# Optimization experiments

Hardware: AMD Instinct MI355X
Metric: run time of the kernel (lower is better)

Reference implementation:

```python
import jax, jax.numpy as jnp
from jax import lax
import numpy as np

D_MODEL = 768
D_STATE = 64
D_CONV = 4
EXPAND = 2
HEADDIM = 128
NGROUPS = 1
D_INNER = EXPAND * D_MODEL            # 1536
NHEADS = D_INNER // HEADDIM           # 12
D_IN_PROJ = 2 * D_INNER + 2 * NGROUPS * D_STATE + NHEADS  # 3212
CONV_DIM = D_INNER + 2 * NGROUPS * D_STATE                # 1664
BATCH, SEQLEN = 2, 4096
EPS = 1e-5


def setup_inputs() -> dict:
    key = jax.random.key(0)
    ks = jax.random.split(key, 8)
    u = jax.random.normal(ks[0], (BATCH, SEQLEN, D_MODEL), jnp.float32)
    W_in = jax.random.normal(ks[1], (D_IN_PROJ, D_MODEL), jnp.float32) * 0.02
    conv_w = jax.random.normal(ks[2], (CONV_DIM, D_CONV), jnp.float32) * 0.2
    conv_b = jnp.zeros((CONV_DIM,), jnp.float32)
    # dt_bias init as in BaseMambaBlock: inv-softplus of dt ~ logU(dt_min, dt_max)
    dt = jnp.exp(jax.random.uniform(ks[3], (NHEADS,)) * (np.log(0.1) - np.log(0.001)) + np.log(0.001))
    dt = jnp.clip(dt, 1e-4, None)
    dt_bias = dt + jnp.log(-jnp.expm1(-dt))
    A_log = jnp.log(jnp.abs(jax.random.normal(ks[4], (NHEADS,), jnp.float32)))
    Dp = jnp.ones((NHEADS,), jnp.float32)
    norm_w = jnp.ones((D_INNER,), jnp.float32)
    W_out = jax.random.normal(ks[5], (D_MODEL, D_INNER), jnp.float32) * 0.02
    return dict(u=u, W_in=W_in, conv_w=conv_w, conv_b=conv_b, dt_bias=dt_bias,
                A_log=A_log, Dp=Dp, norm_w=norm_w, W_out=W_out)


def _silu(x):
    return x * jax.nn.sigmoid(x)


def _depthwise_causal_conv(x, w, b):
    # x: [B, L, C], w: [C, W], b: [C]. Causal: left-pad W-1, crop to L.
    Bt, L, C = x.shape
    xp = jnp.pad(x, ((0, 0), (D_CONV - 1, 0), (0, 0)))
    # stack D_CONV shifted views: [B, L, C, W]
    taps = jnp.stack([xp[:, k:k + L, :] for k in range(D_CONV)], axis=-1)
    return jnp.einsum('blcw,cw->blc', taps, w) + b


def reference(u, W_in, conv_w, conv_b, dt_bias, A_log, Dp, norm_w, W_out):
    Bt, L, _ = u.shape
    zxbcdt = jnp.einsum('bld,ed->ble', u, W_in)  # [B, L, 3212]
    z = zxbcdt[..., :D_INNER]                                   # [B,L,1536]
    xBC = zxbcdt[..., D_INNER:D_INNER + CONV_DIM]               # [B,L,1664]
    dt = zxbcdt[..., D_INNER + CONV_DIM:]                       # [B,L,H]
    dt = jax.nn.softplus(dt + dt_bias)                          # [B,L,H]

    xBC = _silu(_depthwise_causal_conv(xBC, conv_w, conv_b))
    x = xBC[..., :D_INNER].reshape(Bt, L, NHEADS, HEADDIM)      # [B,L,H,P]
    Bm = xBC[..., D_INNER:D_INNER + NGROUPS * D_STATE]          # [B,L,N] (ngroups=1)
    Cm = xBC[..., D_INNER + NGROUPS * D_STATE:]                 # [B,L,N]

    A = -jnp.exp(A_log)                                         # [H]
    dA = jnp.exp(dt * A)                                        # [B,L,H]

    # time-major scan over the selective-state-space recurrence
    xs = (jnp.swapaxes(x, 0, 1),   # [L,B,H,P]
          jnp.swapaxes(dt, 0, 1),  # [L,B,H]
          jnp.swapaxes(dA, 0, 1),  # [L,B,H]
          jnp.swapaxes(Bm, 0, 1),  # [L,B,N]
          jnp.swapaxes(Cm, 0, 1))  # [L,B,N]

    def step(state, inp):
        x_t, dt_t, dA_t, B_t, C_t = inp
        # state: [B,H,P,N]
        state = state * dA_t[..., None, None] + (dt_t[..., None] * x_t)[..., None] * B_t[:, None, None, :]
        y_t = jnp.einsum('bhpn,bn->bhp', state, C_t)
        return state, y_t

    state0 = jnp.zeros((Bt, NHEADS, HEADDIM, D_STATE), u.dtype)
    _, y = lax.scan(step, state0, xs)                           # y: [L,B,H,P]
    y = jnp.swapaxes(y, 0, 1) + Dp[None, None, :, None] * x     # skip term D*x
    y = y.reshape(Bt, L, D_INNER)

    # RMSNormGated, norm_before_gate=False: normalize(y * silu(z)) * weight
    g = y * _silu(z)
    g = g * jax.lax.rsqrt(jnp.mean(g * g, axis=-1, keepdims=True) + EPS) * norm_w
    return jnp.einsum('bli,di->bld', g, W_out)
```

## Files before the change

### kernel.cpp

```cpp
#include <hip/hip_runtime.h>
#include <hip/hip_bf16.h>
#include <stdint.h>

#define BATCH   2
#define SEQLEN  4096
#define DMODEL  768
#define DSTATE  64
#define DCONV   4
#define HEADDIM 128
#define NHEADS  12
#define DINNER  1536
#define DINPROJ 3212
#define CONVDIM 1664
#define DXBC    1676
#define NPAD1   3328
#define ROWS    (BATCH*SEQLEN)
#define CHUNK   64
#define NCHUNK  (SEQLEN/CHUNK)
#define CROWS   8
#define TBUF    4096

typedef __bf16 bf16x8 __attribute__((ext_vector_type(8)));
typedef float  f32x4  __attribute__((ext_vector_type(4)));

__device__ __forceinline__ f32x4 splat4(float v) { return (f32x4){v, v, v, v}; }

__device__ __forceinline__ void load_lds16(const void* g, void* l) {
    __builtin_amdgcn_global_load_lds(
        (const __attribute__((address_space(1))) unsigned int*)g,
        (__attribute__((address_space(3))) unsigned int*)l, 16, 0, 0);
}

__global__ void cvt_bf16_kernel(const float* __restrict__ src,
                                __hip_bfloat16* __restrict__ dst, int n) {
    int i = (blockIdx.x * blockDim.x + threadIdx.x) * 4;
    if (i + 3 < n) {
        float4 v = *(const float4*)(src + i);
        dst[i + 0] = __float2bfloat16(v.x);
        dst[i + 1] = __float2bfloat16(v.y);
        dst[i + 2] = __float2bfloat16(v.z);
        dst[i + 3] = __float2bfloat16(v.w);
    } else {
        for (; i < n; ++i) dst[i] = __float2bfloat16(src[i]);
    }
}

__global__ void padw1_kernel(const float* __restrict__ src,
                             __hip_bfloat16* __restrict__ dst) {
    int i = blockIdx.x * blockDim.x + threadIdx.x;
    if (i >= NPAD1 * DMODEL) return;
    int r = i / DMODEL;
    float v = (r < DINPROJ) ? src[i] : 0.f;
    dst[i] = __float2bfloat16(v);
}

__global__ __launch_bounds__(256) void gemm_bf16_nt(
    const __hip_bfloat16* __restrict__ A,
    const __hip_bfloat16* __restrict__ Bt,
    float* __restrict__ C,
    int M, int Nreal, int K, int ldc)
{
    __shared__ __align__(16) __hip_bfloat16 As[2 * TBUF];
    __shared__ __align__(16) __hip_bfloat16 Bs[2 * TBUF];
    const int tid  = threadIdx.x;
    const int lane = tid & 63;
    const int wave = tid >> 6;
    const int wm   = wave >> 1;
    const int wn   = wave & 1;
    const int tm   = blockIdx.x * 128;
    const int tn   = blockIdx.y * 128;

    f32x4 acc[4][4] = {};

    const int lrow = tid >> 2;
    const int lk8s = ((tid & 3) * 8) ^ (((tid >> 3) & 3) << 3);
    const __hip_bfloat16* gA0 = A  + (size_t)(tm + lrow)      * K + lk8s;
    const __hip_bfloat16* gA1 = A  + (size_t)(tm + lrow + 64) * K + lk8s;
    const __hip_bfloat16* gB0 = Bt + (size_t)(tn + lrow)      * K + lk8s;
    const __hip_bfloat16* gB1 = Bt + (size_t)(tn + lrow + 64) * K + lk8s;

    const int fr  = lane & 15;
    const int fks = ((lane >> 4) * 8) ^ (((lane >> 1) & 3) << 3);

    load_lds16(gA0, As + tid * 8);
    load_lds16(gA1, As + tid * 8 + 2048);
    load_lds16(gB0, Bs + tid * 8);
    load_lds16(gB1, Bs + tid * 8 + 2048);
    __syncthreads();

    int bufo = 0;
    for (int kk = 0; kk < K; kk += 32) {
        const int nbufo = bufo ^ TBUF;
        if (kk + 32 < K) {
            load_lds16(gA0 + kk + 32, As + nbufo + tid * 8);
            load_lds16(gA1 + kk + 32, As + nbufo + tid * 8 + 2048);
            load_lds16(gB0 + kk + 32, Bs + nbufo + tid * 8);
            load_lds16(gB1 + kk + 32, Bs + nbufo + tid * 8 + 2048);
        }
        bf16x8 af[4], bfr[4];
#pragma unroll
        for (int i = 0; i < 4; ++i) {
            af[i]  = *(const bf16x8*)(As + bufo + (wm * 64 + i * 16 + fr) * 32 + fks);
            bfr[i] = *(const bf16x8*)(Bs + bufo + (wn * 64 + i * 16 + fr) * 32 + fks);
        }
#pragma unroll
        for (int mi = 0; mi < 4; ++mi)
#pragma unroll
            for (int ni = 0; ni < 4; ++ni)
                acc[mi][ni] = __builtin_amdgcn_mfma_f32_16x16x32_bf16(
                    af[mi], bfr[ni], acc[mi][ni], 0, 0, 0);
        __syncthreads();
        bufo = nbufo;
    }

    const int rq = (lane >> 4) * 4;
#pragma unroll
    for (int mi = 0; mi < 4; ++mi) {
#pragma unroll
        for (int ni = 0; ni < 4; ++ni) {
            int col = tn + wn * 64 + ni * 16 + fr;
            if (col < Nreal) {
                size_t rbase = (size_t)(tm + wm * 64 + mi * 16 + rq) * ldc + col;
#pragma unroll
                for (int j = 0; j < 4; ++j)
                    C[rbase + (size_t)j * ldc] = acc[mi][ni][j];
            }
        }
    }
}

__global__ __launch_bounds__(256) void gemm1_fused(
    const __hip_bfloat16* __restrict__ A,
    const __hip_bfloat16* __restrict__ Bt,
    float* __restrict__ Cz,
    float* __restrict__ Cx)
{
    __shared__ __align__(16) __hip_bfloat16 As[2 * TBUF];
    __shared__ __align__(16) __hip_bfloat16 Bs[2 * TBUF];
    const int tid  = threadIdx.x;
    const int lane = tid & 63;
    const int wave = tid >> 6;
    const int wm   = wave >> 1;
    const int wn   = wave & 1;
    const int tm   = blockIdx.x * 128;
    const int tn   = blockIdx.y * 128;
    const int K    = DMODEL;

    float* Co;
    int ldc2, cb, nb;
    if (tn < DINNER) { Co = Cz; ldc2 = DINNER; cb = tn;          nb = DINNER; }
    else             { Co = Cx; ldc2 = DXBC;   cb = tn - DINNER; nb = DXBC;   }

    f32x4 acc[4][4] = {};

    const int lrow = tid >> 2;
    const int lk8s = ((tid & 3) * 8) ^ (((tid >> 3) & 3) << 3);
    const __hip_bfloat16* gA0 = A  + (size_t)(tm + lrow)      * K + lk8s;
    const __hip_bfloat16* gA1 = A  + (size_t)(tm + lrow + 64) * K + lk8s;
    const __hip_bfloat16* gB0 = Bt + (size_t)(tn + lrow)      * K + lk8s;
    const __hip_bfloat16* gB1 = Bt + (size_t)(tn + lrow + 64) * K + lk8s;

    const int fr  = lane & 15;
    const int fks = ((lane >> 4) * 8) ^ (((lane >> 1) & 3) << 3);

    load_lds16(gA0, As + tid * 8);
    load_lds16(gA1, As + tid * 8 + 2048);
    load_lds16(gB0, Bs + tid * 8);
    load_lds16(gB1, Bs + tid * 8 + 2048);
    __syncthreads();

    int bufo = 0;
    for (int kk = 0; kk < K; kk += 32) {
        const int nbufo = bufo ^ TBUF;
        if (kk + 32 < K) {
            load_lds16(gA0 + kk + 32, As + nbufo + tid * 8);
            load_lds16(gA1 + kk + 32, As + nbufo + tid * 8 + 2048);
            load_lds16(gB0 + kk + 32, Bs + nbufo + tid * 8);
            load_lds16(gB1 + kk + 32, Bs + nbufo + tid * 8 + 2048);
        }
        bf16x8 af[4], bfr[4];
#pragma unroll
        for (int i = 0; i < 4; ++i) {
            af[i]  = *(const bf16x8*)(As + bufo + (wm * 64 + i * 16 + fr) * 32 + fks);
            bfr[i] = *(const bf16x8*)(Bs + bufo + (wn * 64 + i * 16 + fr) * 32 + fks);
        }
#pragma unroll
        for (int mi = 0; mi < 4; ++mi)
#pragma unroll
            for (int ni = 0; ni < 4; ++ni)
                acc[mi][ni] = __builtin_amdgcn_mfma_f32_16x16x32_bf16(
                    af[mi], bfr[ni], acc[mi][ni], 0, 0, 0);
        __syncthreads();
        bufo = nbufo;
    }

    const int rq = (lane >> 4) * 4;
#pragma unroll
    for (int mi = 0; mi < 4; ++mi) {
#pragma unroll
        for (int ni = 0; ni < 4; ++ni) {
            int col = cb + wn * 64 + ni * 16 + fr;
            if (col < nb) {
                size_t rbase = (size_t)(tm + wm * 64 + mi * 16 + rq) * ldc2 + col;
#pragma unroll
                for (int j = 0; j < 4; ++j)
                    Co[rbase + (size_t)j * ldc2] = acc[mi][ni][j];
            }
        }
    }
}

__global__ void conv_kernel(const float* __restrict__ xbcdt,
                            const float* __restrict__ convw,
                            const float* __restrict__ convb,
                            float* __restrict__ xbuf,
                            float* __restrict__ Bm,
                            float* __restrict__ Cm)
{
    int c = blockIdx.x * 256 + threadIdx.x;
    if (c >= CONVDIM) return;
    size_t row0 = (size_t)blockIdx.y * CROWS;
    int l0 = (int)(row0 & (SEQLEN - 1));
    float w0 = convw[c * 4 + 0];
    float w1 = convw[c * 4 + 1];
    float w2 = convw[c * 4 + 2];
    float w3 = convw[c * 4 + 3];
    float bias = convb[c];
    const float* src = xbcdt + row0 * DXBC + c;
    float x0 = (l0 >= 3) ? src[-3 * DXBC] : 0.f;
    float x1 = (l0 >= 2) ? src[-2 * DXBC] : 0.f;
    float x2 = (l0 >= 1) ? src[-1 * DXBC] : 0.f;
#pragma unroll
    for (int r = 0; r < CROWS; ++r) {
        float x3 = src[(size_t)r * DXBC];
        float acc = bias + x0 * w0 + x1 * w1 + x2 * w2 + x3 * w3;
        float v = acc / (1.f + __expf(-acc));
        size_t row = row0 + r;
        if (c < DINNER)               xbuf[row * DINNER + c] = v;
        else if (c < DINNER + DSTATE) Bm[row * DSTATE + (c - DINNER)] = v;
        else                          Cm[row * DSTATE + (c - DINNER - DSTATE)] = v;
        x0 = x1; x1 = x2; x2 = x3;
    }
}

__global__ void dt_kernel(const float* __restrict__ xbcdt,
                          const float* __restrict__ dt_bias,
                          const float* __restrict__ A_log,
                          float* __restrict__ dtb, float* __restrict__ dAb)
{
    int i = blockIdx.x * 256 + threadIdx.x;
    if (i >= ROWS * NHEADS) return;
    int row = i / NHEADS, h = i - row * NHEADS;
    float v = xbcdt[(size_t)row * DXBC + CONVDIM + h] + dt_bias[h];
    float dt = (v > 20.f) ? v : log1pf(__expf(v));
    float A = -__expf(A_log[h]);
    dtb[i] = dt;
    dAb[i] = __expf(dt * A);
}

__global__ __launch_bounds__(256) void chunk_state_f32(
    const float* __restrict__ xbuf, const float* __restrict__ Bm,
    const float* __restrict__ dtb, const float* __restrict__ dAb,
    float* __restrict__ Sloc, float* __restrict__ Pk)
{
    const int blk = blockIdx.x;
    const int k   = blk % NCHUNK;
    const int bh  = blk / NCHUNK;
    const int h   = bh % NHEADS;
    const int b   = bh / NHEADS;
    const int tid = threadIdx.x;
    const int pg  = tid >> 3;
    const int n0  = (tid & 7) * 8;
    const size_t row0 = (size_t)b * SEQLEN + k * CHUNK;
    const float* xbase = xbuf + (row0 * NHEADS + h) * HEADDIM + pg * 4;

    __shared__ __align__(16) float lB[CHUNK][DSTATE];
    __shared__ float lDA[CHUNK];
    __shared__ float ldt[CHUNK];

    for (int i = tid; i < CHUNK * DSTATE / 4; i += 256)
        ((float4*)&lB[0][0])[i] = ((const float4*)(Bm + row0 * DSTATE))[i];
    if (tid < CHUNK) {
        lDA[tid] = dAb[(row0 + tid) * NHEADS + h];
        ldt[tid] = dtb[(row0 + tid) * NHEADS + h];
    }
    __syncthreads();

    f32x4 s4[4][2] = {};
    f32x4 xt0[4], xt1[4];

#pragma unroll
    for (int tt = 0; tt < 4; ++tt)
        xt0[tt] = *(const f32x4*)(xbase + (size_t)tt * (NHEADS * HEADDIM));

#pragma unroll
    for (int tile = 0; tile < 16; ++tile) {
        f32x4* cur = (tile & 1) ? xt1 : xt0;
        f32x4* nxt = (tile & 1) ? xt0 : xt1;
        if (tile < 15) {
#pragma unroll
            for (int tt = 0; tt < 4; ++tt)
                nxt[tt] = *(const f32x4*)(xbase +
                    (size_t)((tile + 1) * 4 + tt) * (NHEADS * HEADDIM));
        }
#pragma unroll
        for (int tt = 0; tt < 4; ++tt) {
            int t = tile * 4 + tt;
            f32x4 da4 = splat4(lDA[t]);
            float dtv = ldt[t];
            f32x4 bv0 = *(const f32x4*)&lB[t][n0];
            f32x4 bv1 = *(const f32x4*)&lB[t][n0 + 4];
#pragma unroll
            for (int pl = 0; pl < 4; ++pl) {
                f32x4 dtx = splat4(dtv * cur[tt][pl]);
                s4[pl][0] = s4[pl][0] * da4 + dtx * bv0;
                s4[pl][1] = s4[pl][1] * da4 + dtx * bv1;
            }
        }
    }

    const size_t kbase = (size_t)(bh * NCHUNK + k) * (HEADDIM * DSTATE);
#pragma unroll
    for (int pl = 0; pl < 4; ++pl) {
        size_t a = kbase + (size_t)(pg * 4 + pl) * DSTATE + n0;
        *(f32x4*)(Sloc + a)     = s4[pl][0];
        *(f32x4*)(Sloc + a + 4) = s4[pl][1];
    }

    if (tid == 0) {
        float pr = 1.f;
#pragma unroll 8
        for (int t = 0; t < CHUNK; ++t) pr *= lDA[t];
        Pk[bh * NCHUNK + k] = pr;
    }
}

__global__ __launch_bounds__(256) void scan_phase2(
    float* __restrict__ Sloc, const float* __restrict__ Pk)
{
    int bh = blockIdx.x >> 5;
    int eo = (blockIdx.x & 31) * 256 + threadIdx.x;
    __shared__ float lP[NCHUNK];
    if (threadIdx.x < NCHUNK) lP[threadIdx.x] = Pk[bh * NCHUNK + threadIdx.x];
    __syncthreads();
    float s = 0.f;
    size_t base = (size_t)bh * NCHUNK * 8192 + eo;
#pragma unroll 8
    for (int k = 0; k < NCHUNK; ++k) {
        size_t a = base + (size_t)k * 8192;
        float f = Sloc[a];
        Sloc[a] = s;
        s = s * lP[k] + f;
    }
}

__global__ __launch_bounds__(256) void chunk_y_f32(
    const float* __restrict__ xbuf, const float* __restrict__ Bm,
    const float* __restrict__ Cm, const float* __restrict__ dtb,
    const float* __restrict__ dAb, const float* __restrict__ Dp,
    const float* __restrict__ Sini, float* __restrict__ ybuf)
{
    const int blk = blockIdx.x;
    const int kp  = blk % (NCHUNK / 2);
    const int bh  = blk / (NCHUNK / 2);
    const int h   = bh % NHEADS;
    const int b   = bh / NHEADS;
    const int tid = threadIdx.x;
    const int sub = tid >> 7;
    const int t2  = tid & 127;
    const int pg  = t2 >> 2;
    const int q   = t2 & 3;
    const int n0  = q * 16;
    const size_t prow0 = (size_t)b * SEQLEN + (size_t)kp * 2 * CHUNK;
    const size_t row0  = prow0 + (size_t)sub * CHUNK;
    const float* xbase = xbuf + (row0 * NHEADS + h) * HEADDIM + pg * 4;
    float* ybase = ybuf + (row0 * NHEADS + h) * HEADDIM + pg * 4;

    __shared__ __align__(16) float lB[64][DSTATE];
    __shared__ __align__(16) float lC[64][DSTATE];
    __shared__ float lDA[2 * CHUNK];
    __shared__ float ldt[2 * CHUNK];

    if (tid < 2 * CHUNK) {
        lDA[tid] = dAb[(prow0 + tid) * NHEADS + h];
        ldt[tid] = dtb[(prow0 + tid) * NHEADS + h];
    }

    f32x4 s4[4][4];
    const size_t kbase = (size_t)(bh * NCHUNK + kp * 2 + sub) * (HEADDIM * DSTATE);
#pragma unroll
    for (int pl = 0; pl < 4; ++pl) {
        size_t a = kbase + (size_t)(pg * 4 + pl) * DSTATE + n0;
#pragma unroll
        for (int nq = 0; nq < 4; ++nq)
            s4[pl][nq] = *(const f32x4*)(Sini + a + nq * 4);
    }
    const float dph = Dp[h];

#pragma unroll
    for (int w = 0; w < 2; ++w) {
        for (int i = tid; i < 64 * DSTATE / 4; i += 256) {
            int r  = i >> 4;
            int c4 = i & 15;
            size_t gr = prow0 + (size_t)(r >> 5) * CHUNK + w * 32 + (r & 31);
            ((float4*)&lB[r][0])[c4] = ((const float4*)(Bm + gr * DSTATE))[c4];
            ((float4*)&lC[r][0])[c4] = ((const float4*)(Cm + gr * DSTATE))[c4];
        }
        __syncthreads();

        f32x4 xt0[4], xt1[4];
#pragma unroll
        for (int tt = 0; tt < 4; ++tt)
            xt0[tt] = *(const f32x4*)(xbase + (size_t)(w * 32 + tt) * (NHEADS * HEADDIM));

#pragma unroll
        for (int tile = 0; tile < 8; ++tile) {
            f32x4* cur = (tile & 1) ? xt1 : xt0;
            f32x4* nxt = (tile & 1) ? xt0 : xt1;
            if (tile < 7) {
#pragma unroll
                for (int tt = 0; tt < 4; ++tt)
                    nxt[tt] = *(const f32x4*)(xbase +
                        (size_t)(w * 32 + (tile + 1) * 4 + tt) * (NHEADS * HEADDIM));
            }
#pragma unroll
            for (int tt = 0; tt < 4; ++tt) {
                int t  = w * 32 + tile * 4 + tt;
                int tr = sub * 32 + tile * 4 + tt;
                f32x4 da4 = splat4(lDA[sub * CHUNK + t]);
                float dtv = ldt[sub * CHUNK + t];
                f32x4 bv0 = *(const f32x4*)&lB[tr][n0];
                f32x4 bv1 = *(const f32x4*)&lB[tr][n0 + 4];
                f32x4 bv2 = *(const f32x4*)&lB[tr][n0 + 8];
                f32x4 bv3 = *(const f32x4*)&lB[tr][n0 + 12];
                f32x4 cv0 = *(const f32x4*)&lC[tr][n0];
                f32x4 cv1 = *(const f32x4*)&lC[tr][n0 + 4];
                f32x4 cv2 = *(const f32x4*)&lC[tr][n0 + 8];
                f32x4 cv3 = *(const f32x4*)&lC[tr][n0 + 12];
                float yr[4];
#pragma unroll
                for (int pl = 0; pl < 4; ++pl) {
                    f32x4 dtx = splat4(dtv * cur[tt][pl]);
                    f32x4 v0 = s4[pl][0] * da4 + dtx * bv0;
                    f32x4 v1 = s4[pl][1] * da4 + dtx * bv1;
                    f32x4 v2 = s4[pl][2] * da4 + dtx * bv2;
                    f32x4 v3 = s4[pl][3] * da4 + dtx * bv3;
                    s4[pl][0] = v0; s4[pl][1] = v1; s4[pl][2] = v2; s4[pl][3] = v3;
                    f32x4 y4 = cv0 * v0 + cv1 * v1 + cv2 * v2 + cv3 * v3;
                    float y = (y4[0] + y4[1]) + (y4[2] + y4[3]);
                    y += __shfl_xor(y, 1);
                    y += __shfl_xor(y, 2);
                    yr[pl] = y;
                }
                if (q == 0) {
                    f32x4 wv = {yr[0] + dph * cur[tt][0], yr[1] + dph * cur[tt][1],
                                yr[2] + dph * cur[tt][2], yr[3] + dph * cur[tt][3]};
                    *(f32x4*)(ybase + (size_t)t * (NHEADS * HEADDIM)) = wv;
                }
            }
        }
        if (w == 0) __syncthreads();
    }
}

#define NT 64
__global__ __launch_bounds__(256) void scan_kernel(
    const float* __restrict__ xbuf, const float* __restrict__ Bm,
    const float* __restrict__ Cm, const float* __restrict__ dtb,
    const float* __restrict__ dAb, const float* __restrict__ Dp,
    float* __restrict__ ybuf)
{
    int blk = blockIdx.x;
    int ps = blk & 7;
    int h  = (blk >> 3) % NHEADS;
    int b  = blk / (NHEADS * 8);
    int p0 = ps * 16;
    int tid = threadIdx.x;
    int pl  = tid >> 4;
    int n0  = (tid & 15) * 4;

    __shared__ __align__(16) float lB[NT][64];
    __shared__ __align__(16) float lC[NT][64];
    __shared__ __align__(16) float lDtx[NT][16];
    __shared__ float lDA[NT];
    __shared__ float lY[NT][16];

    float s0 = 0.f, s1 = 0.f, s2 = 0.f, s3 = 0.f;
    float dph = Dp[h];
    size_t rowbase = (size_t)b * SEQLEN;

    for (int t0 = 0; t0 < SEQLEN; t0 += NT) {
        for (int i = tid; i < NT * 64 / 4; i += 256) {
            ((float4*)&lB[0][0])[i] = ((const float4*)Bm)[(rowbase + t0) * 16 + i];
            ((float4*)&lC[0][0])[i] = ((const float4*)Cm)[(rowbase + t0) * 16 + i];
        }
        for (int i = tid; i < NT * 16; i += 256) {
            int t = i >> 4, pp = i & 15;
            size_t r = rowbase + t0 + t;
            lDtx[t][pp] = dtb[r * NHEADS + h] * xbuf[(r * NHEADS + h) * HEADDIM + p0 + pp];
        }
        if (tid < NT) lDA[tid] = dAb[(rowbase + t0 + tid) * NHEADS + h];
        __syncthreads();

        for (int t = 0; t < NT; ++t) {
            float da  = lDA[t];
            float dtx = lDtx[t][pl];
            const float* bp = &lB[t][n0];
            const float* cp = &lC[t][n0];
            s0 = s0 * da + dtx * bp[0];
            s1 = s1 * da + dtx * bp[1];
            s2 = s2 * da + dtx * bp[2];
            s3 = s3 * da + dtx * bp[3];
            float part = s0 * cp[0] + s1 * cp[1] + s2 * cp[2] + s3 * cp[3];
            part += __shfl_xor(part, 1);
            part += __shfl_xor(part, 2);
            part += __shfl_xor(part, 4);
            part += __shfl_xor(part, 8);
            if ((tid & 15) == 0) lY[t][pl] = part;
        }
        __syncthreads();

        for (int i = tid; i < NT * 16; i += 256) {
            int t = i >> 4, pp = i & 15;
            size_t r = rowbase + t0 + t;
            size_t gi = (r * NHEADS + h) * HEADDIM + p0 + pp;
            ybuf[gi] = lY[t][pp] + dph * xbuf[gi];
        }
        __syncthreads();
    }
}

__global__ __launch_bounds__(256) void gate_rms_kernel(
    const float* __restrict__ ybuf, const float* __restrict__ zbuf,
    const float* __restrict__ norm_w, __hip_bfloat16* __restrict__ gbf)
{
    int row = blockIdx.x;
    int tid = threadIdx.x;
    const float2* y2 = (const float2*)(ybuf + (size_t)row * DINNER);
    const float2* z2 = (const float2*)(zbuf + (size_t)row * DINNER);
    const float2* nw2 = (const float2*)norm_w;
    float g[6];
    float ss = 0.f;
#pragma unroll
    for (int j = 0; j < 3; ++j) {
        int idx = tid + j * 256;
        float2 yy = y2[idx];
        float2 zz = z2[idx];
        float g0 = yy.x * (zz.x / (1.f + __expf(-zz.x)));
        float g1 = yy.y * (zz.y / (1.f + __expf(-zz.y)));
        g[j * 2 + 0] = g0;
        g[j * 2 + 1] = g1;
        ss += g0 * g0 + g1 * g1;
    }
#pragma unroll
    for (int m = 1; m < 64; m <<= 1) ss += __shfl_xor(ss, m);
    __shared__ float red[4];
    if ((tid & 63) == 0) red[tid >> 6] = ss;
    __syncthreads();
    float tot = red[0] + red[1] + red[2] + red[3];
    float scale = rsqrtf(tot * (1.f / DINNER) + 1e-5f);
#pragma unroll
    for (int j = 0; j < 3; ++j) {
        int idx = tid + j * 256;
        float2 w = nw2[idx];
        __hip_bfloat162 o;
        o.x = __float2bfloat16(g[j * 2 + 0] * scale * w.x);
        o.y = __float2bfloat16(g[j * 2 + 1] * scale * w.y);
        *(__hip_bfloat162*)(gbf + (size_t)row * DINNER + idx * 2) = o;
    }
}

extern "C" void kernel_launch(void* const* d_in, const int* in_sizes, int n_in,
                              void* d_out, int out_size, void* d_ws, size_t ws_size,
                              hipStream_t stream)
{
    const float* u       = (const float*)d_in[0];
    const float* W_in    = (const float*)d_in[1];
    const float* conv_w  = (const float*)d_in[2];
    const float* conv_b  = (const float*)d_in[3];
    const float* dt_bias = (const float*)d_in[4];
    const float* A_log   = (const float*)d_in[5];
    const float* Dp      = (const float*)d_in[6];
    const float* norm_w  = (const float*)d_in[7];
    const float* W_out   = (const float*)d_in[8];
    float* out = (float*)d_out;

    char* ws = (char*)d_ws;
    size_t off = 0;
    auto alloc = [&](size_t bytes) {
        char* p = ws + off;
        off += (bytes + 255) & ~(size_t)255;
        return p;
    };
    __hip_bfloat16* ubf  = (__hip_bfloat16*)alloc((size_t)ROWS * DMODEL * 2);
    __hip_bfloat16* W1bf = (__hip_bfloat16*)alloc((size_t)NPAD1 * DMODEL * 2);
    __hip_bfloat16* W2bf = (__hip_bfloat16*)alloc((size_t)DMODEL * DINNER * 2);
    float* zbuf  = (float*)alloc((size_t)ROWS * DINNER * 4);
    float* xbcdt = (float*)alloc((size_t)ROWS * DXBC * 4);
    float* xbuf = (float*)alloc((size_t)ROWS * DINNER * 4);
    float* Bmb  = (float*)alloc((size_t)ROWS * DSTATE * 4);
    float* Cmb  = (float*)alloc((size_t)ROWS * DSTATE * 4);
    float* dtb  = (float*)alloc((size_t)ROWS * NHEADS * 4);
    float* dAb  = (float*)alloc((size_t)ROWS * NHEADS * 4);
    float* ybuf = (float*)alloc((size_t)ROWS * DINNER * 4);
    float* Pkb  = (float*)alloc((size_t)BATCH * NHEADS * NCHUNK * 4);
    __hip_bfloat16* gbf = (__hip_bfloat16*)xbuf;
    float* Sloc = (float*)xbcdt;
    bool chunked = (off <= ws_size);

    cvt_bf16_kernel<<<(ROWS * DMODEL / 4 + 255) / 256, 256, 0, stream>>>(u, ubf, ROWS * DMODEL);
    padw1_kernel<<<(NPAD1 * DMODEL + 255) / 256, 256, 0, stream>>>(W_in, W1bf);
    cvt_bf16_kernel<<<(DMODEL * DINNER / 4 + 255) / 256, 256, 0, stream>>>(W_out, W2bf, DMODEL * DINNER);

    gemm1_fused<<<dim3(ROWS / 128, NPAD1 / 128), 256, 0, stream>>>(
        ubf, W1bf, zbuf, xbcdt);

    conv_kernel<<<dim3((CONVDIM + 255) / 256, ROWS / CROWS), 256, 0, stream>>>(
        xbcdt, conv_w, conv_b, xbuf, Bmb, Cmb);

    dt_kernel<<<(ROWS * NHEADS + 255) / 256, 256, 0, stream>>>(xbcdt, dt_bias, A_log, dtb, dAb);

    if (chunked) {
        chunk_state_f32<<<BATCH * NHEADS * NCHUNK, 256, 0, stream>>>(
            xbuf, Bmb, dtb, dAb, Sloc, Pkb);
        scan_phase2<<<BATCH * NHEADS * 32, 256, 0, stream>>>(Sloc, Pkb);
        chunk_y_f32<<<BATCH * NHEADS * NCHUNK / 2, 256, 0, stream>>>(
            xbuf, Bmb, Cmb, dtb, dAb, Dp, Sloc, ybuf);
    } else {
        scan_kernel<<<BATCH * NHEADS * 8, 256, 0, stream>>>(
            xbuf, Bmb, Cmb, dtb, dAb, Dp, ybuf);
    }

    gate_rms_kernel<<<ROWS, 256, 0, stream>>>(ybuf, zbuf, norm_w, gbf);

    gemm_bf16_nt<<<dim3(ROWS / 128, DMODEL / 128), 256, 0, stream>>>(
        gbf, W2bf, out, ROWS, DMODEL, DINNER, DMODEL);
}
```

Measured before the change: 305.3 us.

## Fuse dt computation into conv kernel and give each chunk its own block in chunk_y

```diff
diff --git a/kernel.cpp b/kernel.cpp
--- a/kernel.cpp
+++ b/kernel.cpp
@@ -213,49 +213,52 @@
 __global__ void conv_kernel(const float* __restrict__ xbcdt,
                             const float* __restrict__ convw,
                             const float* __restrict__ convb,
+                            const float* __restrict__ dt_bias,
+                            const float* __restrict__ A_log,
                             float* __restrict__ xbuf,
                             float* __restrict__ Bm,
-                            float* __restrict__ Cm)
+                            float* __restrict__ Cm,
+                            float* __restrict__ dtb,
+                            float* __restrict__ dAb)
 {
     int c = blockIdx.x * 256 + threadIdx.x;
-    if (c >= CONVDIM) return;
     size_t row0 = (size_t)blockIdx.y * CROWS;
-    int l0 = (int)(row0 & (SEQLEN - 1));
-    float w0 = convw[c * 4 + 0];
-    float w1 = convw[c * 4 + 1];
-    float w2 = convw[c * 4 + 2];
-    float w3 = convw[c * 4 + 3];
-    float bias = convb[c];
-    const float* src = xbcdt + row0 * DXBC + c;
-    float x0 = (l0 >= 3) ? src[-3 * DXBC] : 0.f;
-    float x1 = (l0 >= 2) ? src[-2 * DXBC] : 0.f;
-    float x2 = (l0 >= 1) ? src[-1 * DXBC] : 0.f;
-#pragma unroll
-    for (int r = 0; r < CROWS; ++r) {
-        float x3 = src[(size_t)r * DXBC];
-        float acc = bias + x0 * w0 + x1 * w1 + x2 * w2 + x3 * w3;
-        float v = acc / (1.f + __expf(-acc));
-        size_t row = row0 + r;
-        if (c < DINNER)               xbuf[row * DINNER + c] = v;
-        else if (c < DINNER + DSTATE) Bm[row * DSTATE + (c - DINNER)] = v;
-        else                          Cm[row * DSTATE + (c - DINNER - DSTATE)] = v;
-        x0 = x1; x1 = x2; x2 = x3;
-    }
-}
-
-__global__ void dt_kernel(const float* __restrict__ xbcdt,
-                          const float* __restrict__ dt_bias,
-                          const float* __restrict__ A_log,
-                          float* __restrict__ dtb, float* __restrict__ dAb)
-{
-    int i = blockIdx.x * 256 + threadIdx.x;
-    if (i >= ROWS * NHEADS) return;
-    int row = i / NHEADS, h = i - row * NHEADS;
-    float v = xbcdt[(size_t)row * DXBC + CONVDIM + h] + dt_bias[h];
-    float dt = (v > 20.f) ? v : log1pf(__expf(v));
-    float A = -__expf(A_log[h]);
-    dtb[i] = dt;
-    dAb[i] = __expf(dt * A);
+    if (c < CONVDIM) {
+        int l0 = (int)(row0 & (SEQLEN - 1));
+        float w0 = convw[c * 4 + 0];
+        float w1 = convw[c * 4 + 1];
+        float w2 = convw[c * 4 + 2];
+        float w3 = convw[c * 4 + 3];
+        float bias = convb[c];
+        const float* src = xbcdt + row0 * DXBC + c;
+        float x0 = (l0 >= 3) ? src[-3 * DXBC] : 0.f;
+        float x1 = (l0 >= 2) ? src[-2 * DXBC] : 0.f;
+        float x2 = (l0 >= 1) ? src[-1 * DXBC] : 0.f;
+#pragma unroll
+        for (int r = 0; r < CROWS; ++r) {
+            float x3 = src[(size_t)r * DXBC];
+            float acc = bias + x0 * w0 + x1 * w1 + x2 * w2 + x3 * w3;
+            float v = acc / (1.f + __expf(-acc));
+            size_t row = row0 + r;
+            if (c < DINNER)               xbuf[row * DINNER + c] = v;
+            else if (c < DINNER + DSTATE) Bm[row * DSTATE + (c - DINNER)] = v;
+            else                          Cm[row * DSTATE + (c - DINNER - DSTATE)] = v;
+            x0 = x1; x1 = x2; x2 = x3;
+        }
+    } else if (c < DXBC) {
+        int h = c - CONVDIM;
+        float bias = dt_bias[h];
+        float A = -__expf(A_log[h]);
+        const float* src = xbcdt + row0 * DXBC + c;
+#pragma unroll
+        for (int r = 0; r < CROWS; ++r) {
+            float v = src[(size_t)r * DXBC] + bias;
+            float dt = (v > 20.f) ? v : log1pf(__expf(v));
+            size_t row = row0 + r;
+            dtb[row * NHEADS + h] = dt;
+            dAb[row * NHEADS + h] = __expf(dt * A);
+        }
+    }
 }
 
 __global__ __launch_bounds__(256) void chunk_state_f32(
@@ -361,105 +364,96 @@
     const float* __restrict__ Sini, float* __restrict__ ybuf)
 {
     const int blk = blockIdx.x;
-    const int kp  = blk % (NCHUNK / 2);
-    const int bh  = blk / (NCHUNK / 2);
+    const int k   = blk % NCHUNK;
+    const int bh  = blk / NCHUNK;
     const int h   = bh % NHEADS;
     const int b   = bh / NHEADS;
     const int tid = threadIdx.x;
-    const int sub = tid >> 7;
-    const int t2  = tid & 127;
-    const int pg  = t2 >> 2;
-    const int q   = t2 & 3;
+    const int pg  = tid >> 2;
+    const int q   = tid & 3;
     const int n0  = q * 16;
-    const size_t prow0 = (size_t)b * SEQLEN + (size_t)kp * 2 * CHUNK;
-    const size_t row0  = prow0 + (size_t)sub * CHUNK;
-    const float* xbase = xbuf + (row0 * NHEADS + h) * HEADDIM + pg * 4;
-    float* ybase = ybuf + (row0 * NHEADS + h) * HEADDIM + pg * 4;
-
-    __shared__ __align__(16) float lB[64][DSTATE];
-    __shared__ __align__(16) float lC[64][DSTATE];
-    __shared__ float lDA[2 * CHUNK];
-    __shared__ float ldt[2 * CHUNK];
-
-    if (tid < 2 * CHUNK) {
-        lDA[tid] = dAb[(prow0 + tid) * NHEADS + h];
-        ldt[tid] = dtb[(prow0 + tid) * NHEADS + h];
-    }
-
-    f32x4 s4[4][4];
-    const size_t kbase = (size_t)(bh * NCHUNK + kp * 2 + sub) * (HEADDIM * DSTATE);
-#pragma unroll
-    for (int pl = 0; pl < 4; ++pl) {
-        size_t a = kbase + (size_t)(pg * 4 + pl) * DSTATE + n0;
+    const size_t row0 = (size_t)b * SEQLEN + k * CHUNK;
+    const float* xbase = xbuf + (row0 * NHEADS + h) * HEADDIM + pg * 2;
+    float* ybase = ybuf + (row0 * NHEADS + h) * HEADDIM + pg * 2;
+
+    __shared__ __align__(16) float lB[CHUNK][DSTATE];
+    __shared__ __align__(16) float lC[CHUNK][DSTATE];
+    __shared__ float lDA[CHUNK];
+    __shared__ float ldt[CHUNK];
+
+    for (int i = tid; i < CHUNK * DSTATE / 4; i += 256) {
+        ((float4*)&lB[0][0])[i] = ((const float4*)(Bm + row0 * DSTATE))[i];
+        ((float4*)&lC[0][0])[i] = ((const float4*)(Cm + row0 * DSTATE))[i];
+    }
+    if (tid < CHUNK) {
+        lDA[tid] = dAb[(row0 + tid) * NHEADS + h];
+        ldt[tid] = dtb[(row0 + tid) * NHEADS + h];
+    }
+
+    f32x4 s4[2][4];
+    const size_t kbase = (size_t)(bh * NCHUNK + k) * (HEADDIM * DSTATE);
+#pragma unroll
+    for (int pl = 0; pl < 2; ++pl) {
+        size_t a = kbase + (size_t)(pg * 2 + pl) * DSTATE + n0;
 #pragma unroll
         for (int nq = 0; nq < 4; ++nq)
             s4[pl][nq] = *(const f32x4*)(Sini + a + nq * 4);
     }
     const float dph = Dp[h];
 
-#pragma unroll
-    for (int w = 0; w < 2; ++w) {
-        for (int i = tid; i < 64 * DSTATE / 4; i += 256) {
-            int r  = i >> 4;
-            int c4 = i & 15;
-            size_t gr = prow0 + (size_t)(r >> 5) * CHUNK + w * 32 + (r & 31);
-            ((float4*)&lB[r][0])[c4] = ((const float4*)(Bm + gr * DSTATE))[c4];
-            ((float4*)&lC[r][0])[c4] = ((const float4*)(Cm + gr * DSTATE))[c4];
-        }
-        __syncthreads();
-
-        f32x4 xt0[4], xt1[4];
-#pragma unroll
-        for (int tt = 0; tt < 4; ++tt)
-            xt0[tt] = *(const f32x4*)(xbase + (size_t)(w * 32 + tt) * (NHEADS * HEADDIM));
-
-#pragma unroll
-        for (int tile = 0; tile < 8; ++tile) {
-            f32x4* cur = (tile & 1) ? xt1 : xt0;
-            f32x4* nxt = (tile & 1) ? xt0 : xt1;
-            if (tile < 7) {
-#pragma unroll
-                for (int tt = 0; tt < 4; ++tt)
-                    nxt[tt] = *(const f32x4*)(xbase +
-                        (size_t)(w * 32 + (tile + 1) * 4 + tt) * (NHEADS * HEADDIM));
+    float xa[2][8], xb[2][8];
+#pragma unroll
+    for (int tt = 0; tt < 8; ++tt) {
+        float2 v = *(const float2*)(xbase + (size_t)tt * (NHEADS * HEADDIM));
+        xa[0][tt] = v.x; xa[1][tt] = v.y;
+    }
+    __syncthreads();
+
+#pragma unroll
+    for (int tile = 0; tile < 8; ++tile) {
+        float (*cur)[8] = (tile & 1) ? xb : xa;
+        float (*nxt)[8] = (tile & 1) ? xa : xb;
+        if (tile < 7) {
+#pragma unroll
+            for (int tt = 0; tt < 8; ++tt) {
+                float2 v = *(const float2*)(xbase +
+                    (size_t)((tile + 1) * 8 + tt) * (NHEADS * HEADDIM));
+                nxt[0][tt] = v.x; nxt[1][tt] = v.y;
             }
-#pragma unroll
-            for (int tt = 0; tt < 4; ++tt) {
-                int t  = w * 32 + tile * 4 + tt;
-                int tr = sub * 32 + tile * 4 + tt;
-                f32x4 da4 = splat4(lDA[sub * CHUNK + t]);
-                float dtv = ldt[sub * CHUNK + t];
-                f32x4 bv0 = *(const f32x4*)&lB[tr][n0];
-                f32x4 bv1 = *(const f32x4*)&lB[tr][n0 + 4];
-                f32x4 bv2 = *(const f32x4*)&lB[tr][n0 + 8];
-                f32x4 bv3 = *(const f32x4*)&lB[tr][n0 + 12];
-                f32x4 cv0 = *(const f32x4*)&lC[tr][n0];
-                f32x4 cv1 = *(const f32x4*)&lC[tr][n0 + 4];
-                f32x4 cv2 = *(const f32x4*)&lC[tr][n0 + 8];
-                f32x4 cv3 = *(const f32x4*)&lC[tr][n0 + 12];
-                float yr[4];
-#pragma unroll
-                for (int pl = 0; pl < 4; ++pl) {
-                    f32x4 dtx = splat4(dtv * cur[tt][pl]);
-                    f32x4 v0 = s4[pl][0] * da4 + dtx * bv0;
-                    f32x4 v1 = s4[pl][1] * da4 + dtx * bv1;
-                    f32x4 v2 = s4[pl][2] * da4 + dtx * bv2;
-                    f32x4 v3 = s4[pl][3] * da4 + dtx * bv3;
-                    s4[pl][0] = v0; s4[pl][1] = v1; s4[pl][2] = v2; s4[pl][3] = v3;
-                    f32x4 y4 = cv0 * v0 + cv1 * v1 + cv2 * v2 + cv3 * v3;
-                    float y = (y4[0] + y4[1]) + (y4[2] + y4[3]);
-                    y += __shfl_xor(y, 1);
-                    y += __shfl_xor(y, 2);
-                    yr[pl] = y;
-                }
-                if (q == 0) {
-                    f32x4 wv = {yr[0] + dph * cur[tt][0], yr[1] + dph * cur[tt][1],
-                                yr[2] + dph * cur[tt][2], yr[3] + dph * cur[tt][3]};
-                    *(f32x4*)(ybase + (size_t)t * (NHEADS * HEADDIM)) = wv;
-                }
+        }
+#pragma unroll
+        for (int tt = 0; tt < 8; ++tt) {
+            int t = tile * 8 + tt;
+            f32x4 da4 = splat4(lDA[t]);
+            float dtv = ldt[t];
+            f32x4 bv0 = *(const f32x4*)&lB[t][n0];
+            f32x4 bv1 = *(const f32x4*)&lB[t][n0 + 4];
+            f32x4 bv2 = *(const f32x4*)&lB[t][n0 + 8];
+            f32x4 bv3 = *(const f32x4*)&lB[t][n0 + 12];
+            f32x4 cv0 = *(const f32x4*)&lC[t][n0];
+            f32x4 cv1 = *(const f32x4*)&lC[t][n0 + 4];
+            f32x4 cv2 = *(const f32x4*)&lC[t][n0 + 8];
+            f32x4 cv3 = *(const f32x4*)&lC[t][n0 + 12];
+            float yr[2];
+#pragma unroll
+            for (int pl = 0; pl < 2; ++pl) {
+                f32x4 dtx = splat4(dtv * cur[pl][tt]);
+                f32x4 v0 = s4[pl][0] * da4 + dtx * bv0;
+                f32x4 v1 = s4[pl][1] * da4 + dtx * bv1;
+                f32x4 v2 = s4[pl][2] * da4 + dtx * bv2;
+                f32x4 v3 = s4[pl][3] * da4 + dtx * bv3;
+                s4[pl][0] = v0; s4[pl][1] = v1; s4[pl][2] = v2; s4[pl][3] = v3;
+                f32x4 y4 = cv0 * v0 + cv1 * v1 + cv2 * v2 + cv3 * v3;
+                float y = (y4[0] + y4[1]) + (y4[2] + y4[3]);
+                y += __shfl_xor(y, 1);
+                y += __shfl_xor(y, 2);
+                yr[pl] = y;
             }
-        }
-        if (w == 0) __syncthreads();
+            if (q == 0) {
+                float2 w = {yr[0] + dph * cur[0][tt], yr[1] + dph * cur[1][tt]};
+                *(float2*)(ybase + (size_t)t * (NHEADS * HEADDIM)) = w;
+            }
+        }
     }
 }
 
@@ -615,16 +609,14 @@
     gemm1_fused<<<dim3(ROWS / 128, NPAD1 / 128), 256, 0, stream>>>(
         ubf, W1bf, zbuf, xbcdt);
 
-    conv_kernel<<<dim3((CONVDIM + 255) / 256, ROWS / CROWS), 256, 0, stream>>>(
-        xbcdt, conv_w, conv_b, xbuf, Bmb, Cmb);
-
-    dt_kernel<<<(ROWS * NHEADS + 255) / 256, 256, 0, stream>>>(xbcdt, dt_bias, A_log, dtb, dAb);
+    conv_kernel<<<dim3((DXBC + 255) / 256, ROWS / CROWS), 256, 0, stream>>>(
+        xbcdt, conv_w, conv_b, dt_bias, A_log, xbuf, Bmb, Cmb, dtb, dAb);
 
     if (chunked) {
         chunk_state_f32<<<BATCH * NHEADS * NCHUNK, 256, 0, stream>>>(
             xbuf, Bmb, dtb, dAb, Sloc, Pkb);
         scan_phase2<<<BATCH * NHEADS * 32, 256, 0, stream>>>(Sloc, Pkb);
-        chunk_y_f32<<<BATCH * NHEADS * NCHUNK / 2, 256, 0, stream>>>(
+        chunk_y_f32<<<BATCH * NHEADS * NCHUNK, 256, 0, stream>>>(
             xbuf, Bmb, Cmb, dtb, dAb, Dp, Sloc, ybuf);
     } else {
         scan_kernel<<<BATCH * NHEADS * 8, 256, 0, stream>>>(
```

New measurement: 296.1 us. 1.03x faster.
